# Optimization experiments

Hardware: AMD Instinct MI355X
Metric: run time of the kernel (lower is better)

The kernel has to match this reference:

```python
import jax, jax.numpy as jnp
import numpy as np

B, D, K = 4, 128, 512   # batch, node_embedding_dim, num_nodes
ALPHA = 0.2             # LeakyReLU negative slope


def setup_inputs() -> dict:
    key = jax.random.key(0)
    k1, k2, k3, k4 = jax.random.split(key, 4)
    x = jax.random.normal(k1, (B, D, K), dtype=jnp.float32)
    # nn.Linear(2D -> D): store weight as (2D, D) for right-multiplication
    lin_w = jax.random.normal(k2, (2 * D, D), dtype=jnp.float32) * (1.0 / np.sqrt(2 * D))
    lin_b = jax.random.normal(k3, (D,), dtype=jnp.float32) * 0.01
    # attention vector a: (D,) (xavier-uniform in torch; scale-equivalent normal here)
    a = jax.random.normal(k4, (D,), dtype=jnp.float32) * (1.414 * np.sqrt(2.0 / (D + 1)))
    bias_mat = jnp.zeros((K, K), dtype=jnp.float32)  # init zeros per module
    return {"x": x, "lin_w": lin_w, "lin_b": lin_b, "a": a, "bias_mat": bias_mat}


def reference(x, lin_w, lin_b, a, bias_mat):
    # x: (B, D, K) -> transpose to (B, K, D); GATv2 path, residual = identity
    xt = jnp.swapaxes(x, 1, 2)                      # (B, K, D)
    d = xt.shape[-1]
    # lin(concat(v_i, v_j)) == v_i @ W1 + v_j @ W2 + b  (exact split; avoids (B,K,K,2D) concat)
    W1, W2 = lin_w[:d], lin_w[d:]
    left = xt @ W1 + lin_b                          # (B, K, D) -- v_i part (repeating block)
    right = xt @ W2                                 # (B, K, D) -- v_j part (alternating block)
    pre = left[:, :, None, :] + right[:, None, :, :]  # (B, K, K, D)
    h = jnp.where(pre > 0, pre, ALPHA * pre)        # LeakyReLU
    e = jnp.einsum('bijd,d->bij', h, a) + bias_mat  # (B, K, K)
    attn = jax.nn.softmax(e, axis=2)                # softmax over j (dropout p=0)
    agg = jnp.einsum('bij,bjd->bid', attn, xt)      # (B, K, D)
    out = jax.nn.sigmoid(agg) + xt                  # sigmoid + identity residual
    return jnp.swapaxes(out, 1, 2)                  # (B, D, K)
```

## Files before the change

### kernel.cpp

```cpp
#include <hip/hip_runtime.h>

#define B 4
#define D 128
#define K 512
#define TI 8

__global__ __launch_bounds__(128) void gat_rhat(const float* __restrict__ x,
                                                const float* __restrict__ lin_w,
                                                const float* __restrict__ a,
                                                float* __restrict__ Rt) {
  const int j0 = blockIdx.x * 128;
  const int e0 = blockIdx.y * 8;
  const int b = blockIdx.z;
  const int t = threadIdx.x;
  __shared__ float sw2[D][8];
#pragma unroll
  for (int u = 0; u < 8; ++u) {
    const int idx = u * 128 + t;
    sw2[idx >> 3][idx & 7] =
        lin_w[(size_t)(D + (idx >> 3)) * D + e0 + (idx & 7)];
  }
  __syncthreads();
  float acc[8];
#pragma unroll
  for (int u = 0; u < 8; ++u) acc[u] = 0.f;
  const float* xcol = x + (size_t)b * D * K + j0 + t;
#pragma unroll 8
  for (int c = 0; c < D; ++c) {
    const float xv = xcol[(size_t)c * K];
    const float4 w0 = *(const float4*)&sw2[c][0];
    const float4 w1 = *(const float4*)&sw2[c][4];
    acc[0] = fmaf(xv, w0.x, acc[0]);
    acc[1] = fmaf(xv, w0.y, acc[1]);
    acc[2] = fmaf(xv, w0.z, acc[2]);
    acc[3] = fmaf(xv, w0.w, acc[3]);
    acc[4] = fmaf(xv, w1.x, acc[4]);
    acc[5] = fmaf(xv, w1.y, acc[5]);
    acc[6] = fmaf(xv, w1.z, acc[6]);
    acc[7] = fmaf(xv, w1.w, acc[7]);
  }
#pragma unroll
  for (int u = 0; u < 8; ++u) {
    const float ue = 0.8f * fabsf(a[e0 + u]);
    Rt[((size_t)b * D + e0 + u) * K + j0 + t] = ue * acc[u];
  }
}

__global__ __launch_bounds__(512) void gat_attn2(
    const float* __restrict__ x, const float* __restrict__ lin_w,
    const float* __restrict__ lin_b, const float* __restrict__ a,
    const float* __restrict__ bias, const float* __restrict__ Rt,
    float* __restrict__ out) {
  const int i0 = blockIdx.x * TI;
  const int b = blockIdx.y;
  const int t = threadIdx.x;

  __shared__ float sxt[D][TI];
  __shared__ float sLhat[D][TI];
  __shared__ float ssign[D];
  __shared__ float sSLh[TI];
  __shared__ float spart[64];
  __shared__ float seT[TI][K];

#pragma unroll
  for (int r = 0; r < 2; ++r) {
    const int idx = r * 512 + t;
    sxt[idx >> 3][idx & 7] = x[((size_t)b * D + (idx >> 3)) * K + i0 + (idx & 7)];
  }
  if (t < D) ssign[t] = (a[t] >= 0.f) ? 1.f : -1.f;
  __syncthreads();

  {
    const int e = t & (D - 1);
    const int ig = t >> 7;
    float l0 = 0.f, l1 = 0.f;
    const float* w1p = lin_w + e;
#pragma unroll 8
    for (int c = 0; c < D; ++c) {
      const float w = w1p[(size_t)c * D];
      const float2 xv = *(const float2*)&sxt[c][2 * ig];
      l0 = fmaf(xv.x, w, l0);
      l1 = fmaf(xv.y, w, l1);
    }
    const float ue = 0.8f * fabsf(a[e]);
    const float bv = lin_b[e];
    sLhat[e][2 * ig] = ue * (l0 + bv);
    sLhat[e][2 * ig + 1] = ue * (l1 + bv);
  }
  __syncthreads();
  if (t < 64) {
    const int ii = t >> 3, seg = t & 7;
    float p = 0.f;
#pragma unroll
    for (int d = seg * 16; d < seg * 16 + 16; ++d)
      p = fmaf(ssign[d], sLhat[d][ii], p);
    spart[t] = p;
  }
  __syncthreads();
  if (t < TI) {
    float s = 0.f;
#pragma unroll
    for (int g = 0; g < 8; ++g) s += spart[t * 8 + g];
    sSLh[t] = s;
  }
  __syncthreads();

  {
    float acc[8];
#pragma unroll
    for (int ii = 0; ii < 8; ++ii) acc[ii] = 0.f;
    float sR = 0.f;
    const float* rcol = Rt + (size_t)b * D * K + t;
#pragma unroll 4
    for (int d = 0; d < D; ++d) {
      const float rv = rcol[(size_t)d * K];
      const float sg = ssign[d];
      float lh[8];
      *(float4*)&lh[0] = *(const float4*)&sLhat[d][0];
      *(float4*)&lh[4] = *(const float4*)&sLhat[d][4];
      sR = fmaf(sg, rv, sR);
#pragma unroll
      for (int ii = 0; ii < 8; ++ii) {
        const float p = lh[ii] + rv;
        acc[ii] = fmaf(sg, fmaxf(p, 0.f), acc[ii]);
      }
    }
#pragma unroll
    for (int ii = 0; ii < 8; ++ii)
      seT[ii][t] = acc[ii] + 0.25f * (sSLh[ii] + sR) +
                   bias[(size_t)(i0 + ii) * K + t];
  }
  __syncthreads();

  {
    const int w = t >> 6, lane = t & 63;
    float v[8];
    float m = -1e30f;
#pragma unroll
    for (int q = 0; q < 8; ++q) {
      v[q] = seT[w][lane + 64 * q];
      m = fmaxf(m, v[q]);
    }
#pragma unroll
    for (int off = 32; off > 0; off >>= 1) m = fmaxf(m, __shfl_xor(m, off, 64));
    float s = 0.f;
#pragma unroll
    for (int q = 0; q < 8; ++q) {
      v[q] = __expf(v[q] - m);
      s += v[q];
    }
#pragma unroll
    for (int off = 32; off > 0; off >>= 1) s += __shfl_xor(s, off, 64);
    const float inv = 1.f / s;
#pragma unroll
    for (int q = 0; q < 8; ++q) seT[w][lane + 64 * q] = v[q] * inv;
  }
  __syncthreads();

  {
    const int dg = t >> 2, jg = t & 3;
    float ag[8];
#pragma unroll
    for (int ii = 0; ii < 8; ++ii) ag[ii] = 0.f;
    const float4* xr = (const float4*)(x + ((size_t)b * D + dg) * K);
#pragma unroll 2
    for (int q = 0; q < 32; ++q) {
      const int chunk = q * 4 + jg;
      const float4 xv = xr[chunk];
#pragma unroll
      for (int ii = 0; ii < 8; ++ii) {
        const float4 av = ((const float4*)&seT[ii][0])[chunk];
        ag[ii] = fmaf(av.x, xv.x, ag[ii]);
        ag[ii] = fmaf(av.y, xv.y, ag[ii]);
        ag[ii] = fmaf(av.z, xv.z, ag[ii]);
        ag[ii] = fmaf(av.w, xv.w, ag[ii]);
      }
    }
#pragma unroll
    for (int ii = 0; ii < 8; ++ii) {
      ag[ii] += __shfl_xor(ag[ii], 1, 64);
      ag[ii] += __shfl_xor(ag[ii], 2, 64);
    }
#pragma unroll
    for (int r = 0; r < 2; ++r) {
      const int ii = jg + 4 * r;
      const float sg = 1.f / (1.f + __expf(-ag[ii]));
      out[((size_t)b * D + dg) * K + i0 + ii] = sg + sxt[dg][ii];
    }
  }
}

#define ALPHA 0.2f
__global__ __launch_bounds__(512) void gat_fused(
    const float* __restrict__ x, const float* __restrict__ lin_w,
    const float* __restrict__ lin_b, const float* __restrict__ a,
    const float* __restrict__ bias, float* __restrict__ out) {
  const int i = blockIdx.x, b = blockIdx.y, t = threadIdx.x;
  __shared__ float sxi[D], sLi[D], sa[D];
  __shared__ float lpart[4 * D];
  __shared__ float xtT[D * 64];
  __shared__ float epars[8 * 64];
  __shared__ float se[K];
  __shared__ float sattn[K], spart[K];
  __shared__ float sred[8];

  if (t < D) {
    sxi[t] = x[((size_t)b * D + t) * K + i];
    sa[t] = a[t];
  }
  __syncthreads();
  {
    const int c = t & (D - 1), q = t >> 7;
    float acc = 0.f;
    const float* W1 = lin_w + c;
#pragma unroll 8
    for (int d = q * 32; d < q * 32 + 32; ++d)
      acc = fmaf(sxi[d], W1[(size_t)d * D], acc);
    lpart[q * D + c] = acc;
  }
  __syncthreads();
  if (t < D)
    sLi[t] = lin_b[t] + lpart[t] + lpart[D + t] + lpart[2 * D + t] +
             lpart[3 * D + t];
  __syncthreads();

  for (int jt = 0; jt < K / 64; ++jt) {
    const int j0 = jt * 64;
    for (int idx = t; idx < D * 64; idx += 512)
      xtT[idx] = x[((size_t)b * D + (idx >> 6)) * K + j0 + (idx & 63)];
    __syncthreads();
    const int jj = t & 63, g = t >> 6, dp0 = g * 16;
    float accv[16];
#pragma unroll
    for (int v = 0; v < 16; ++v) accv[v] = 0.f;
    for (int dc = 0; dc < D; dc += 16) {
      float xv[16];
#pragma unroll
      for (int u = 0; u < 16; ++u) xv[u] = xtT[(dc + u) * 64 + jj];
#pragma unroll
      for (int u = 0; u < 16; ++u) {
        const float* W2r = lin_w + (size_t)(D + dc + u) * D + dp0;
#pragma unroll
        for (int v = 0; v < 16; ++v) accv[v] = fmaf(xv[u], W2r[v], accv[v]);
      }
    }
    float ep = 0.f;
#pragma unroll
    for (int v = 0; v < 16; ++v) {
      const float pre = sLi[dp0 + v] + accv[v];
      ep = fmaf(sa[dp0 + v], pre > 0.f ? pre : ALPHA * pre, ep);
    }
    epars[g * 64 + jj] = ep;
    __syncthreads();
    if (t < 64) {
      float esum = bias[(size_t)i * K + j0 + t];
#pragma unroll
      for (int g2 = 0; g2 < 8; ++g2) esum += epars[g2 * 64 + t];
      se[j0 + t] = esum;
    }
    __syncthreads();
  }

  float e = se[t];
  float m = e;
#pragma unroll
  for (int off = 32; off > 0; off >>= 1) m = fmaxf(m, __shfl_xor(m, off, 64));
  if ((t & 63) == 0) sred[t >> 6] = m;
  __syncthreads();
  m = sred[0];
#pragma unroll
  for (int w = 1; w < 8; ++w) m = fmaxf(m, sred[w]);
  const float ev = __expf(e - m);
  float s = ev;
#pragma unroll
  for (int off = 32; off > 0; off >>= 1) s += __shfl_xor(s, off, 64);
  __syncthreads();
  if ((t & 63) == 0) sred[t >> 6] = s;
  __syncthreads();
  s = 0.f;
#pragma unroll
  for (int w = 0; w < 8; ++w) s += sred[w];
  sattn[t] = ev * (1.f / s);
  __syncthreads();

  const int d = t >> 2, c = t & 3;
  const float4* X4 = (const float4*)(x + ((size_t)b * D + d) * K);
  const float4* A4 = (const float4*)sattn;
  float p = 0.f;
#pragma unroll 4
  for (int q = 0; q < K / 16; ++q) {
    const int idx = c + 4 * q;
    float4 xv = X4[idx], av = A4[idx];
    p = fmaf(av.x, xv.x, p);
    p = fmaf(av.y, xv.y, p);
    p = fmaf(av.z, xv.z, p);
    p = fmaf(av.w, xv.w, p);
  }
  spart[t] = p;
  __syncthreads();
  if (t < D) {
    const float agg =
        spart[4 * t] + spart[4 * t + 1] + spart[4 * t + 2] + spart[4 * t + 3];
    const float sg = 1.f / (1.f + __expf(-agg));
    out[((size_t)b * D + t) * K + i] = sg + sxi[t];
  }
}

extern "C" void kernel_launch(void* const* d_in, const int* in_sizes, int n_in,
                              void* d_out, int out_size, void* d_ws,
                              size_t ws_size, hipStream_t stream) {
  const float* x = (const float*)d_in[0];
  const float* lin_w = (const float*)d_in[1];
  const float* lin_b = (const float*)d_in[2];
  const float* a = (const float*)d_in[3];
  const float* bias = (const float*)d_in[4];
  float* out = (float*)d_out;

  const size_t need = (size_t)B * K * D * sizeof(float);
  if (ws_size >= need && d_ws != nullptr) {
    float* Rt = (float*)d_ws;
    gat_rhat<<<dim3(K / 128, D / 8, B), 128, 0, stream>>>(x, lin_w, a, Rt);
    gat_attn2<<<dim3(K / TI, B), 512, 0, stream>>>(x, lin_w, lin_b, a, bias,
                                                   Rt, out);
  } else {
    gat_fused<<<dim3(K, B), 512, 0, stream>>>(x, lin_w, lin_b, a, bias, out);
  }
}
```

Measured before the change: 98.47 us.

## Use packed fp16 dot2 for pairwise attention scores and precompute both projections

Both linear projections (left and right) are now computed in a single pre-kernel and stored as packed fp16 pairs. The attention kernel's O(K^2·D) inner loop then uses packed half adds, relu and v_dot2 accumulation into fp32. The point is to halve workspace traffic and roughly double ALU throughput on the hot loop. The attention kernel also moves to 4 rows per block with 256 threads, and the redundant per-block W1 matmul is removed. The cost is fp16 rounding (round-toward-zero) in the scores, which may affect accuracy.

```diff
diff --git a/kernel.cpp b/kernel.cpp
--- a/kernel.cpp
+++ b/kernel.cpp
@@ -3,132 +3,163 @@
 #define B 4
 #define D 128
 #define K 512
-#define TI 8
-
-__global__ __launch_bounds__(128) void gat_rhat(const float* __restrict__ x,
-                                                const float* __restrict__ lin_w,
-                                                const float* __restrict__ a,
-                                                float* __restrict__ Rt) {
-  const int j0 = blockIdx.x * 128;
-  const int e0 = blockIdx.y * 8;
+#define TI 4
+
+typedef __fp16 h2v __attribute__((ext_vector_type(2)));
+
+__device__ __forceinline__ unsigned pkrtz(float a, float b) {
+  h2v h = __builtin_amdgcn_cvt_pkrtz(a, b);
+  union { h2v h; unsigned u; } c; c.h = h; return c.u;
+}
+__device__ __forceinline__ h2v u2h(unsigned u) {
+  union { unsigned u; h2v h; } c; c.u = u; return c.h;
+}
+__device__ __forceinline__ float fdot2f(h2v a, h2v b, float c) {
+#if __has_builtin(__builtin_amdgcn_fdot2)
+  return __builtin_amdgcn_fdot2(a, b, c, false);
+#else
+  return c + (float)a.x * (float)b.x + (float)a.y * (float)b.y;
+#endif
+}
+__device__ __forceinline__ h2v relu2(h2v a) {
+#if __has_builtin(__builtin_elementwise_max)
+  const h2v z = {(__fp16)0.f, (__fp16)0.f};
+  return __builtin_elementwise_max(a, z);
+#else
+  h2v r;
+  r.x = (float)a.x > 0.f ? a.x : (__fp16)0.f;
+  r.y = (float)a.y > 0.f ? a.y : (__fp16)0.f;
+  return r;
+#endif
+}
+
+__global__ __launch_bounds__(256) void gat_lr16(
+    const float* __restrict__ x, const float* __restrict__ lin_w,
+    const float* __restrict__ lin_b, const float* __restrict__ a,
+    unsigned* __restrict__ LhT, unsigned* __restrict__ RhT) {
+  const int j0 = blockIdx.x * 64;
+  const int E0 = blockIdx.y * 16;
   const int b = blockIdx.z;
   const int t = threadIdx.x;
-  __shared__ float sw2[D][8];
-#pragma unroll
-  for (int u = 0; u < 8; ++u) {
-    const int idx = u * 128 + t;
-    sw2[idx >> 3][idx & 7] =
-        lin_w[(size_t)(D + (idx >> 3)) * D + e0 + (idx & 7)];
-  }
-  __syncthreads();
-  float acc[8];
-#pragma unroll
-  for (int u = 0; u < 8; ++u) acc[u] = 0.f;
-  const float* xcol = x + (size_t)b * D * K + j0 + t;
+  __shared__ float sx[D][64];
+  __shared__ float sw1[D][16];
+  __shared__ float sw2[D][16];
+#pragma unroll
+  for (int r = 0; r < 8; ++r) {
+    const int fid = t + 256 * r;
+    const int row = fid >> 4, c4 = fid & 15;
+    *(float4*)&sx[row][4 * c4] =
+        *(const float4*)&x[((size_t)b * D + row) * K + j0 + 4 * c4];
+  }
+#pragma unroll
+  for (int r = 0; r < 8; ++r) {
+    const int idx = t + 256 * r;
+    const int row = idx >> 4, e = idx & 15;
+    sw1[row][e] = lin_w[(size_t)row * D + E0 + e];
+    sw2[row][e] = lin_w[(size_t)(D + row) * D + E0 + e];
+  }
+  __syncthreads();
+  const int j = t & 63, g = t >> 6;
+  float accL[4] = {0.f, 0.f, 0.f, 0.f}, accR[4] = {0.f, 0.f, 0.f, 0.f};
 #pragma unroll 8
   for (int c = 0; c < D; ++c) {
-    const float xv = xcol[(size_t)c * K];
-    const float4 w0 = *(const float4*)&sw2[c][0];
-    const float4 w1 = *(const float4*)&sw2[c][4];
-    acc[0] = fmaf(xv, w0.x, acc[0]);
-    acc[1] = fmaf(xv, w0.y, acc[1]);
-    acc[2] = fmaf(xv, w0.z, acc[2]);
-    acc[3] = fmaf(xv, w0.w, acc[3]);
-    acc[4] = fmaf(xv, w1.x, acc[4]);
-    acc[5] = fmaf(xv, w1.y, acc[5]);
-    acc[6] = fmaf(xv, w1.z, acc[6]);
-    acc[7] = fmaf(xv, w1.w, acc[7]);
-  }
-#pragma unroll
-  for (int u = 0; u < 8; ++u) {
-    const float ue = 0.8f * fabsf(a[e0 + u]);
-    Rt[((size_t)b * D + e0 + u) * K + j0 + t] = ue * acc[u];
-  }
-}
-
-__global__ __launch_bounds__(512) void gat_attn2(
-    const float* __restrict__ x, const float* __restrict__ lin_w,
-    const float* __restrict__ lin_b, const float* __restrict__ a,
-    const float* __restrict__ bias, const float* __restrict__ Rt,
-    float* __restrict__ out) {
+    const float xv = sx[c][j];
+    const float4 w1 = *(const float4*)&sw1[c][4 * g];
+    const float4 w2 = *(const float4*)&sw2[c][4 * g];
+    accL[0] = fmaf(xv, w1.x, accL[0]);
+    accL[1] = fmaf(xv, w1.y, accL[1]);
+    accL[2] = fmaf(xv, w1.z, accL[2]);
+    accL[3] = fmaf(xv, w1.w, accL[3]);
+    accR[0] = fmaf(xv, w2.x, accR[0]);
+    accR[1] = fmaf(xv, w2.y, accR[1]);
+    accR[2] = fmaf(xv, w2.z, accR[2]);
+    accR[3] = fmaf(xv, w2.w, accR[3]);
+  }
+  const int e0 = E0 + 4 * g;
+#pragma unroll
+  for (int u = 0; u < 2; ++u) {
+    const int ea = e0 + 2 * u, eb = ea + 1;
+    const float uea = 0.8f * fabsf(a[ea]), ueb = 0.8f * fabsf(a[eb]);
+    const float La = uea * (accL[2 * u] + lin_b[ea]);
+    const float Lb = ueb * (accL[2 * u + 1] + lin_b[eb]);
+    const float Ra = uea * accR[2 * u];
+    const float Rb = ueb * accR[2 * u + 1];
+    const size_t dp = (size_t)(ea >> 1);
+    LhT[((size_t)b * (D / 2) + dp) * K + j0 + j] = pkrtz(La, Lb);
+    RhT[((size_t)b * (D / 2) + dp) * K + j0 + j] = pkrtz(Ra, Rb);
+  }
+}
+
+__global__ __launch_bounds__(256) void gat_attn16(
+    const float* __restrict__ x, const float* __restrict__ a,
+    const float* __restrict__ bias, const unsigned* __restrict__ LhT,
+    const unsigned* __restrict__ RhT, float* __restrict__ out) {
   const int i0 = blockIdx.x * TI;
   const int b = blockIdx.y;
   const int t = threadIdx.x;
-
   __shared__ float sxt[D][TI];
-  __shared__ float sLhat[D][TI];
-  __shared__ float ssign[D];
-  __shared__ float sSLh[TI];
-  __shared__ float spart[64];
+  __shared__ unsigned slh[D / 2][TI];
+  __shared__ unsigned ssg[D / 2];
+  __shared__ float sSL[TI];
   __shared__ float seT[TI][K];
 
-#pragma unroll
-  for (int r = 0; r < 2; ++r) {
-    const int idx = r * 512 + t;
-    sxt[idx >> 3][idx & 7] = x[((size_t)b * D + (idx >> 3)) * K + i0 + (idx & 7)];
-  }
-  if (t < D) ssign[t] = (a[t] >= 0.f) ? 1.f : -1.f;
-  __syncthreads();
-
-  {
-    const int e = t & (D - 1);
-    const int ig = t >> 7;
-    float l0 = 0.f, l1 = 0.f;
-    const float* w1p = lin_w + e;
-#pragma unroll 8
-    for (int c = 0; c < D; ++c) {
-      const float w = w1p[(size_t)c * D];
-      const float2 xv = *(const float2*)&sxt[c][2 * ig];
-      l0 = fmaf(xv.x, w, l0);
-      l1 = fmaf(xv.y, w, l1);
-    }
-    const float ue = 0.8f * fabsf(a[e]);
-    const float bv = lin_b[e];
-    sLhat[e][2 * ig] = ue * (l0 + bv);
-    sLhat[e][2 * ig + 1] = ue * (l1 + bv);
-  }
-  __syncthreads();
-  if (t < 64) {
-    const int ii = t >> 3, seg = t & 7;
-    float p = 0.f;
-#pragma unroll
-    for (int d = seg * 16; d < seg * 16 + 16; ++d)
-      p = fmaf(ssign[d], sLhat[d][ii], p);
-    spart[t] = p;
-  }
-  __syncthreads();
-  if (t < TI) {
-    float s = 0.f;
-#pragma unroll
-    for (int g = 0; g < 8; ++g) s += spart[t * 8 + g];
-    sSLh[t] = s;
-  }
-  __syncthreads();
-
-  {
-    float acc[8];
-#pragma unroll
-    for (int ii = 0; ii < 8; ++ii) acc[ii] = 0.f;
-    float sR = 0.f;
-    const float* rcol = Rt + (size_t)b * D * K + t;
+  {
+    int idx = t;
+    sxt[idx >> 2][idx & 3] = x[((size_t)b * D + (idx >> 2)) * K + i0 + (idx & 3)];
+    idx = t + 256;
+    sxt[idx >> 2][idx & 3] = x[((size_t)b * D + (idx >> 2)) * K + i0 + (idx & 3)];
+    const int dp = t >> 2, ii = t & 3;
+    slh[dp][ii] = LhT[((size_t)b * (D / 2) + dp) * K + i0 + ii];
+    if (t < D / 2) {
+      const float s0 = (a[2 * t] >= 0.f) ? 1.f : -1.f;
+      const float s1 = (a[2 * t + 1] >= 0.f) ? 1.f : -1.f;
+      ssg[t] = pkrtz(s0, s1);
+    }
+  }
+  __syncthreads();
+  {
+    const int ii = t >> 6, dp = t & 63;
+    float v = fdot2f(u2h(ssg[dp]), u2h(slh[dp][ii]), 0.f);
+#pragma unroll
+    for (int off = 32; off > 0; off >>= 1) v += __shfl_xor(v, off, 64);
+    if ((t & 63) == 0) sSL[ii] = v;
+  }
+  __syncthreads();
+
+  {
+    const unsigned* rc = RhT + (size_t)b * (D / 2) * K;
+    float accA[4] = {0.f, 0.f, 0.f, 0.f}, accB[4] = {0.f, 0.f, 0.f, 0.f};
+    float srA = 0.f, srB = 0.f;
 #pragma unroll 4
-    for (int d = 0; d < D; ++d) {
-      const float rv = rcol[(size_t)d * K];
-      const float sg = ssign[d];
-      float lh[8];
-      *(float4*)&lh[0] = *(const float4*)&sLhat[d][0];
-      *(float4*)&lh[4] = *(const float4*)&sLhat[d][4];
-      sR = fmaf(sg, rv, sR);
-#pragma unroll
-      for (int ii = 0; ii < 8; ++ii) {
-        const float p = lh[ii] + rv;
-        acc[ii] = fmaf(sg, fmaxf(p, 0.f), acc[ii]);
-      }
-    }
-#pragma unroll
-    for (int ii = 0; ii < 8; ++ii)
-      seT[ii][t] = acc[ii] + 0.25f * (sSLh[ii] + sR) +
+    for (int dp = 0; dp < D / 2; ++dp) {
+      const unsigned ra = rc[(size_t)dp * K + t];
+      const unsigned rb = rc[(size_t)dp * K + t + 256];
+      const uint4 lh4 = *(const uint4*)&slh[dp][0];
+      const h2v s2 = u2h(ssg[dp]);
+      const h2v rva = u2h(ra), rvb = u2h(rb);
+      srA = fdot2f(s2, rva, srA);
+      srB = fdot2f(s2, rvb, srB);
+      h2v l;
+      l = u2h(lh4.x);
+      accA[0] = fdot2f(s2, relu2(l + rva), accA[0]);
+      accB[0] = fdot2f(s2, relu2(l + rvb), accB[0]);
+      l = u2h(lh4.y);
+      accA[1] = fdot2f(s2, relu2(l + rva), accA[1]);
+      accB[1] = fdot2f(s2, relu2(l + rvb), accB[1]);
+      l = u2h(lh4.z);
+      accA[2] = fdot2f(s2, relu2(l + rva), accA[2]);
+      accB[2] = fdot2f(s2, relu2(l + rvb), accB[2]);
+      l = u2h(lh4.w);
+      accA[3] = fdot2f(s2, relu2(l + rva), accA[3]);
+      accB[3] = fdot2f(s2, relu2(l + rvb), accB[3]);
+    }
+#pragma unroll
+    for (int ii = 0; ii < TI; ++ii) {
+      seT[ii][t] = accA[ii] + 0.25f * (sSL[ii] + srA) +
                    bias[(size_t)(i0 + ii) * K + t];
+      seT[ii][t + 256] = accB[ii] + 0.25f * (sSL[ii] + srB) +
+                         bias[(size_t)(i0 + ii) * K + t + 256];
+    }
   }
   __syncthreads();
 
@@ -158,17 +189,15 @@
   __syncthreads();
 
   {
-    const int dg = t >> 2, jg = t & 3;
-    float ag[8];
-#pragma unroll
-    for (int ii = 0; ii < 8; ++ii) ag[ii] = 0.f;
+    const int dg = t >> 1, jg = t & 1;
+    float ag[4] = {0.f, 0.f, 0.f, 0.f};
     const float4* xr = (const float4*)(x + ((size_t)b * D + dg) * K);
-#pragma unroll 2
-    for (int q = 0; q < 32; ++q) {
-      const int chunk = q * 4 + jg;
+#pragma unroll 4
+    for (int q = 0; q < 64; ++q) {
+      const int chunk = 2 * q + jg;
       const float4 xv = xr[chunk];
 #pragma unroll
-      for (int ii = 0; ii < 8; ++ii) {
+      for (int ii = 0; ii < TI; ++ii) {
         const float4 av = ((const float4*)&seT[ii][0])[chunk];
         ag[ii] = fmaf(av.x, xv.x, ag[ii]);
         ag[ii] = fmaf(av.y, xv.y, ag[ii]);
@@ -177,15 +206,13 @@
       }
     }
 #pragma unroll
-    for (int ii = 0; ii < 8; ++ii) {
-      ag[ii] += __shfl_xor(ag[ii], 1, 64);
-      ag[ii] += __shfl_xor(ag[ii], 2, 64);
-    }
-#pragma unroll
-    for (int r = 0; r < 2; ++r) {
-      const int ii = jg + 4 * r;
-      const float sg = 1.f / (1.f + __expf(-ag[ii]));
-      out[((size_t)b * D + dg) * K + i0 + ii] = sg + sxt[dg][ii];
+    for (int ii = 0; ii < TI; ++ii) ag[ii] += __shfl_xor(ag[ii], 1, 64);
+    if (jg == 0) {
+#pragma unroll
+      for (int ii = 0; ii < TI; ++ii) {
+        const float sg = 1.f / (1.f + __expf(-ag[ii]));
+        out[((size_t)b * D + dg) * K + i0 + ii] = sg + sxt[dg][ii];
+      }
     }
   }
 }
@@ -316,12 +343,14 @@
   const float* bias = (const float*)d_in[4];
   float* out = (float*)d_out;
 
-  const size_t need = (size_t)B * K * D * sizeof(float);
+  const size_t half_words = (size_t)B * (D / 2) * K;
+  const size_t need = 2 * half_words * sizeof(unsigned);
   if (ws_size >= need && d_ws != nullptr) {
-    float* Rt = (float*)d_ws;
-    gat_rhat<<<dim3(K / 128, D / 8, B), 128, 0, stream>>>(x, lin_w, a, Rt);
-    gat_attn2<<<dim3(K / TI, B), 512, 0, stream>>>(x, lin_w, lin_b, a, bias,
-                                                   Rt, out);
+    unsigned* LhT = (unsigned*)d_ws;
+    unsigned* RhT = LhT + half_words;
+    gat_lr16<<<dim3(K / 64, D / 16, B), 256, 0, stream>>>(x, lin_w, lin_b, a,
+                                                          LhT, RhT);
+    gat_attn16<<<dim3(K / TI, B), 256, 0, stream>>>(x, a, bias, LhT, RhT, out);
   } else {
     gat_fused<<<dim3(K, B), 512, 0, stream>>>(x, lin_w, lin_b, a, bias, out);
   }
```

Measured after the change: 87.03 us. 11.6% less time.
